# Kernel tuning notes

Hardware: AMD Instinct MI355X
Metric: run time of the kernel (lower is better)

## Reference

```python
import jax, jax.numpy as jnp
import numpy as np

B, S, H, I, E, TOPK, KS = 4, 4096, 1024, 512, 16, 2, 3


def setup_inputs() -> dict:
    key = jax.random.key(0)
    ks = jax.random.split(key, 9)
    sc = 0.02
    return {
        "hidden_states": jax.random.normal(ks[0], (B, S, H), dtype=jnp.float32),
        "router_w": jax.random.normal(ks[1], (H, E), dtype=jnp.float32) * sc,
        "router_bias": jnp.zeros((E,), dtype=jnp.float32),
        "expert_gate_w": jax.random.normal(ks[2], (E - 1, H, I), dtype=jnp.float32) * sc,
        "expert_up_w": jax.random.normal(ks[3], (E - 1, H, I), dtype=jnp.float32) * sc,
        "expert_down_w": jax.random.normal(ks[4], (E - 1, I, H), dtype=jnp.float32) * sc,
        "conv_w": jax.random.normal(ks[5], (I, H, KS), dtype=jnp.float32) * sc,
        "shared_up_w": jax.random.normal(ks[6], (H, I), dtype=jnp.float32) * sc,
        "shared_down_w": jax.random.normal(ks[7], (I, H), dtype=jnp.float32) * sc,
    }


def reference(hidden_states, router_w, router_bias, expert_gate_w, expert_up_w,
              expert_down_w, conv_w, shared_up_w, shared_down_w):
    b, s, h = hidden_states.shape
    flat = hidden_states.reshape(b * s, h)  # (T, H)

    # ---- Router (mlp type, temperature=1, no noise at eval) ----
    logits = (flat @ router_w).astype(jnp.float32) + router_bias  # (T, E)
    probs = jax.nn.softmax(logits, axis=-1)
    top_w, top_i = jax.lax.top_k(probs, TOPK)  # (T, K)
    norm_w = top_w / (jnp.sum(top_w, axis=-1, keepdims=True) + 1e-6)
    norm_w = norm_w.astype(hidden_states.dtype)
    # Dense combine weights (T, E): scatter top-k weights into expert slots
    combine = jnp.sum(jax.nn.one_hot(top_i, E, dtype=norm_w.dtype) * norm_w[..., None], axis=1)

    # ---- Routed experts: E-1 SwiGLU MLPs + 1 Identity (index E-1) ----
    routed = combine[:, E - 1:E] * flat  # identity expert contribution
    for e in range(E - 1):
        y = (jax.nn.silu(flat @ expert_gate_w[e]) * (flat @ expert_up_w[e])) @ expert_down_w[e]
        routed = routed + combine[:, e:e + 1] * y
    routed = routed.reshape(b, s, h)

    # ---- Shared expert: causal conv1d gate * up, then down ----
    x_ncw = jnp.transpose(hidden_states, (0, 2, 1))  # (B, H, S)
    gate = jax.lax.conv_general_dilated(
        x_ncw, conv_w, window_strides=(1,), padding=[(KS - 1, 0)],
        dimension_numbers=("NCW", "OIW", "NCW"))  # (B, I, S)
    gate = jnp.transpose(gate, (0, 2, 1))  # (B, S, I)
    shared = (jax.nn.silu(gate) * (hidden_states @ shared_up_w)) @ shared_down_w

    return shared + routed
```

## Files before the change

### kernel.cpp

```cpp
#include <hip/hip_runtime.h>

typedef unsigned short u16;
typedef __attribute__((ext_vector_type(4))) float f32x4;
using bf16x8 = __attribute__((ext_vector_type(8))) short;
typedef __attribute__((ext_vector_type(8))) unsigned short u16x8;
typedef __attribute__((ext_vector_type(4))) unsigned short u16x4;

#define GAS __attribute__((address_space(1)))
#define LAS __attribute__((address_space(3)))

__device__ __forceinline__ float bf2f(u16 u) {
  unsigned v = ((unsigned)u) << 16;
  float f;
  __builtin_memcpy(&f, &v, 4);
  return f;
}
__device__ __forceinline__ u16 f2bf(float f) {
  unsigned u;
  __builtin_memcpy(&u, &f, 4);
  u += 0x7fffu + ((u >> 16) & 1u);
  return (u16)(u >> 16);
}
__device__ __forceinline__ void llds16(const void* g, void* l) {
  __builtin_amdgcn_global_load_lds((const GAS unsigned*)g, (LAS unsigned*)l, 16, 0, 0);
}

__global__ void cvtx_k(const float* __restrict__ x, u16* __restrict__ xb) {
  const long i = (long)blockIdx.x * 256 + threadIdx.x;
  f32x4 v = *(const f32x4*)(x + i * 4);
  u16x4 r;
#pragma unroll
  for (int j = 0; j < 4; ++j) r[j] = f2bf(v[j]);
  *(u16x4*)(xb + i * 4) = r;
}

__global__ __launch_bounds__(256) void router_k(const float* __restrict__ x,
    const float* __restrict__ rw, const float* __restrict__ rb,
    int* __restrict__ topk_idx, float* __restrict__ topk_w, int* __restrict__ ib) {
  __shared__ float xs[4][32 * 65];
  __shared__ float wsm[4][32 * 16];
  __shared__ float part[4][64 * 17];
  __shared__ int cnt[16];
  const int tid = threadIdx.x;
  const int wv = __builtin_amdgcn_readfirstlane(tid >> 6);
  const int lane = tid & 63;
  const int tok0 = blockIdx.x * 64;
  const int rr = lane >> 3;
  const int c4 = (lane & 7) * 4;

  float acc[16];
#pragma unroll
  for (int e = 0; e < 16; ++e) acc[e] = 0.f;

  for (int c = 0; c < 8; ++c) {
    const int hb = wv * 256 + c * 32;
    {
      f32x4 wa = *(const f32x4*)(rw + hb * 16 + lane * 4);
      f32x4 wb = *(const f32x4*)(rw + hb * 16 + 256 + lane * 4);
      *(f32x4*)&wsm[wv][lane * 4] = wa;
      *(f32x4*)&wsm[wv][256 + lane * 4] = wb;
    }
#pragma unroll
    for (int i = 0; i < 8; ++i) {
      const int row = i * 8 + rr;
      f32x4 v = *(const f32x4*)(x + (long)(tok0 + row) * 1024 + hb + c4);
#pragma unroll
      for (int j = 0; j < 4; ++j) xs[wv][(c4 + j) * 65 + row] = v[j];
    }
    __syncthreads();
#pragma unroll
    for (int h = 0; h < 32; ++h) {
      const float xv = xs[wv][h * 65 + lane];
      const float* wrow = &wsm[wv][h * 16];
#pragma unroll
      for (int q = 0; q < 4; ++q) {
        f32x4 w4 = *(const f32x4*)(wrow + q * 4);
#pragma unroll
        for (int e = 0; e < 4; ++e) acc[q * 4 + e] += xv * w4[e];
      }
    }
    __syncthreads();
  }
#pragma unroll
  for (int e = 0; e < 16; ++e) part[wv][lane * 17 + e] = acc[e];
  if (tid < 16) cnt[tid] = 0;
  __syncthreads();
  if (tid < 64) {
    float p[16];
#pragma unroll
    for (int e = 0; e < 16; ++e)
      p[e] = part[0][tid * 17 + e] + part[1][tid * 17 + e] +
             part[2][tid * 17 + e] + part[3][tid * 17 + e] + rb[e];
    float mx = p[0];
#pragma unroll
    for (int e = 1; e < 16; ++e) mx = fmaxf(mx, p[e]);
    float sum = 0.f;
#pragma unroll
    for (int e = 0; e < 16; ++e) { p[e] = __expf(p[e] - mx); sum += p[e]; }
    int i0 = 0; float p0 = p[0];
    for (int e = 1; e < 16; ++e) if (p[e] > p0) { p0 = p[e]; i0 = e; }
    int i1 = -1; float p1 = -1.f;
    for (int e = 0; e < 16; ++e) if (e != i0 && p[e] > p1) { p1 = p[e]; i1 = e; }
    const float inv = 1.f / sum;
    p0 *= inv; p1 *= inv;
    const float d = p0 + p1 + 1e-6f;
    const int t = tok0 + tid;
    topk_idx[t * 2] = i0; topk_idx[t * 2 + 1] = i1;
    topk_w[t * 2] = p0 / d;
    topk_w[t * 2 + 1] = p1 / d;
    if (i0 < 15) atomicAdd(&cnt[i0], 1);
    if (i1 < 15) atomicAdd(&cnt[i1], 1);
  }
  __syncthreads();
  if (tid < 15 && cnt[tid] > 0) atomicAdd(&ib[tid], cnt[tid]);
}

__global__ void zero_k(int* __restrict__ ib) {
  if (threadIdx.x < 16) ib[threadIdx.x] = 0;
}

__global__ void scan_k(int* __restrict__ ib) {
  if (threadIdx.x != 0 || blockIdx.x != 0) return;
  int off = 0;
  for (int ee = 0; ee < 15; ++ee) { ib[16 + ee] = off; ib[32 + ee] = off; off += ib[ee]; }
  ib[16 + 15] = off;
  int nm = 0;
  for (int ee = 0; ee < 15; ++ee) {
    const int st = ib[16 + ee], en = ib[16 + ee + 1];
    for (int r = st; r < en; r += 128) {
      ib[64 + nm * 4] = ee; ib[64 + nm * 4 + 1] = r; ib[64 + nm * 4 + 2] = en; ++nm;
    }
  }
  ib[48] = nm;
}

__global__ __launch_bounds__(256) void scatter_k(const int* __restrict__ topk_idx,
                          const float* __restrict__ topk_w,
                          int* __restrict__ ib, int* __restrict__ tok_ids,
                          float* __restrict__ tok_w, int* __restrict__ slot_map) {
  __shared__ int cnt[16], base[16];
  const int tid = threadIdx.x;
  const int j = blockIdx.x * 256 + tid;
  if (tid < 16) cnt[tid] = 0;
  __syncthreads();
  const int e = topk_idx[j];
  int lo = 0;
  if (e < 15) lo = atomicAdd(&cnt[e], 1);
  __syncthreads();
  if (tid < 15 && cnt[tid] > 0) base[tid] = atomicAdd(&ib[32 + tid], cnt[tid]);
  __syncthreads();
  if (e < 15) {
    const int pos = base[e] + lo;
    tok_ids[pos] = j >> 1;
    tok_w[pos] = topk_w[j];
    slot_map[j] = pos;
  } else {
    slot_map[j] = -1;
  }
}

__global__ void transpose_k(const float* __restrict__ src, u16* __restrict__ dst, int R, int C) {
  __shared__ float tile[32][33];
  src += (long)blockIdx.z * R * C;
  dst += (long)blockIdx.z * R * C;
  const int c0 = blockIdx.x * 32, r0 = blockIdx.y * 32;
  const int tx = threadIdx.x & 31, ty = threadIdx.x >> 5;
#pragma unroll
  for (int i = ty; i < 32; i += 8) tile[i][tx] = src[(long)(r0 + i) * C + c0 + tx];
  __syncthreads();
#pragma unroll
  for (int i = ty; i < 32; i += 8) dst[(long)(c0 + i) * R + r0 + tx] = f2bf(tile[tx][i]);
}

__global__ void convt_k(const float* __restrict__ cw, u16* __restrict__ dst) {
  const int idx = blockIdx.x * 256 + threadIdx.x;
  if (idx >= 3 * 512 * 1024) return;
  const int k = idx >> 19;
  const int rem = idx & 524287;
  const int i = rem >> 10, h = rem & 1023;
  dst[idx] = f2bf(cw[i * 3072 + h * 3 + k]);
}

template<int V>
__global__ __launch_bounds__(256, 2)
void gemm_k(const u16* __restrict__ Abase, const u16* __restrict__ Bt0,
            const u16* __restrict__ Bt1, void* __restrict__ OUTv,
            const int* __restrict__ tbl, const int* __restrict__ nmt,
            const int* __restrict__ tok_ids, const float* __restrict__ tok_w,
            int K, int ldA, int ldOut) {
  __shared__ u16 lds[16384];
  u16* OUT = (u16*)OUTv;
  float* OUTF = (float*)OUTv;
  const int tid = threadIdx.x;
  const int wave = tid >> 6, lane = tid & 63;
  const int quad = lane >> 4, l16 = lane & 15;
  const int rA = tid >> 2;
  const int sub8 = (tid & 3) * 8;

  int e = 0, row0, row_end;
  if constexpr (V <= 1) {
    const int mt = blockIdx.x;
    if (mt >= *nmt) return;
    e = tbl[mt * 4]; row0 = tbl[mt * 4 + 1]; row_end = tbl[mt * 4 + 2];
  } else {
    row0 = blockIdx.x * 128; row_end = row0 + 128;
  }
  const int n0 = blockIdx.y * ((V == 0) ? 64 : 128);

  f32x4 acc[2][8];
#pragma unroll
  for (int i = 0; i < 2; ++i)
#pragma unroll
    for (int j = 0; j < 8; ++j) acc[i][j] = (f32x4){0.f, 0.f, 0.f, 0.f};

  const int aoff0 = (wave * 32 + l16) * 32 + quad * 8;
  const int aoff1 = aoff0 + 512;
  u16* ldsA0 = &lds[wave * 512];
  u16* ldsA1 = &lds[2048 + wave * 512];
  u16* ldsB0 = &lds[4096 + wave * 512];
  u16* ldsB1 = &lds[6144 + wave * 512];

  const int nph = (V == 3) ? 3 : 1;
  for (int ph = 0; ph < nph; ++ph) {
    const u16 *pA0, *pA1, *pB0, *pB1;
    bool zero0 = false;
    if constexpr (V == 0) {
      const int t0i = tok_ids[min(row0 + rA, row_end - 1)];
      const int t1i = tok_ids[min(row0 + rA + 64, row_end - 1)];
      pA0 = Abase + (long)t0i * 1024 + sub8;
      pA1 = Abase + (long)t1i * 1024 + sub8;
      pB0 = Bt0 + ((long)e * 512 + n0 + rA) * 1024 + sub8;
      pB1 = Bt1 + ((long)e * 512 + n0 + rA) * 1024 + sub8;
    } else if constexpr (V == 1) {
      pA0 = Abase + (long)min(row0 + rA, row_end - 1) * 512 + sub8;
      pA1 = Abase + (long)min(row0 + rA + 64, row_end - 1) * 512 + sub8;
      pB0 = Bt0 + ((long)e * 1024 + n0 + rA) * 512 + sub8;
      pB1 = Bt0 + ((long)e * 1024 + n0 + rA + 64) * 512 + sub8;
    } else if constexpr (V == 2 || V == 4) {
      pA0 = Abase + (long)(row0 + rA) * ldA + sub8;
      pA1 = Abase + (long)(row0 + rA + 64) * ldA + sub8;
      pB0 = Bt0 + (long)(n0 + rA) * K + sub8;
      pB1 = Bt0 + (long)(n0 + rA + 64) * K + sub8;
    } else {
      const int bb = row0 >> 12, s0 = row0 & 4095;
      const int si0 = s0 + ph - 2 + rA;
      zero0 = si0 < 0;
      pA0 = Abase + ((long)bb * 4096 + (si0 < 0 ? 0 : si0)) * 1024 + sub8;
      pA1 = Abase + ((long)bb * 4096 + (si0 + 64)) * 1024 + sub8;
      pB0 = Bt0 + (long)ph * 512 * 1024 + (long)(n0 + rA) * 1024 + sub8;
      pB1 = Bt0 + (long)ph * 512 * 1024 + (long)(n0 + rA + 64) * 1024 + sub8;
    }
    const int kIters = K / 32;
    for (int kb = 0; kb < kIters; ++kb) {
      u16x8 va0, va1;
      if constexpr (V == 3) {
        va0 = *(const u16x8*)pA0; pA0 += 32;
        va1 = *(const u16x8*)pA1; pA1 += 32;
        if (zero0) va0 = (u16x8){0, 0, 0, 0, 0, 0, 0, 0};
      }
      __syncthreads();
      if constexpr (V == 3) {
        *(u16x8*)&lds[rA * 32 + sub8] = va0;
        *(u16x8*)&lds[(rA + 64) * 32 + sub8] = va1;
      } else {
        llds16(pA0, ldsA0); pA0 += 32;
        llds16(pA1, ldsA1); pA1 += 32;
      }
      llds16(pB0, ldsB0); pB0 += 32;
      llds16(pB1, ldsB1); pB1 += 32;
      __syncthreads();
      bf16x8 a0 = *(const bf16x8*)&lds[aoff0];
      bf16x8 a1 = *(const bf16x8*)&lds[aoff1];
#pragma unroll
      for (int nt = 0; nt < 8; ++nt) {
        bf16x8 b = *(const bf16x8*)&lds[4096 + (nt * 16 + l16) * 32 + quad * 8];
        acc[0][nt] = __builtin_amdgcn_mfma_f32_16x16x32_bf16(a0, b, acc[0][nt], 0, 0, 0);
        acc[1][nt] = __builtin_amdgcn_mfma_f32_16x16x32_bf16(a1, b, acc[1][nt], 0, 0, 0);
      }
    }
  }
  __syncthreads();

  const int rbase = wave * 32;
  if constexpr (V == 0) {
#pragma unroll
    for (int mt = 0; mt < 2; ++mt)
#pragma unroll
      for (int r = 0; r < 4; ++r) {
        const int row = rbase + mt * 16 + quad * 4 + r;
#pragma unroll
        for (int nt = 0; nt < 4; ++nt) {
          float g = acc[mt][nt][r], u = acc[mt][nt + 4][r];
          float sg = g / (1.f + __expf(-g));
          lds[row * 64 + nt * 16 + l16] = f2bf(sg * u);
        }
      }
    __syncthreads();
#pragma unroll
    for (int i = 0; i < 4; ++i) {
      const int c = i * 256 + tid;
      const int row = c >> 3, s8 = (c & 7) * 8;
      const int slot = row0 + row;
      if (slot < row_end)
        *(u16x8*)(OUT + (long)slot * ldOut + n0 + s8) = *(const u16x8*)&lds[row * 64 + s8];
    }
  } else if constexpr (V == 1) {
#pragma unroll
    for (int mt = 0; mt < 2; ++mt)
#pragma unroll
      for (int r = 0; r < 4; ++r) {
        const int row = rbase + mt * 16 + quad * 4 + r;
        const float wgt = tok_w[min(row0 + row, row_end - 1)];
#pragma unroll
        for (int nt = 0; nt < 8; ++nt)
          lds[row * 128 + nt * 16 + l16] = f2bf(acc[mt][nt][r] * wgt);
      }
    __syncthreads();
#pragma unroll
    for (int i = 0; i < 8; ++i) {
      const int c = i * 256 + tid;
      const int row = c >> 4, s8 = (c & 15) * 8;
      const int slot = row0 + row;
      if (slot < row_end)
        *(u16x8*)(OUT + (long)slot * ldOut + n0 + s8) = *(const u16x8*)&lds[row * 128 + s8];
    }
  } else if constexpr (V == 2) {
#pragma unroll
    for (int mt = 0; mt < 2; ++mt)
#pragma unroll
      for (int r = 0; r < 4; ++r) {
        const int row = rbase + mt * 16 + quad * 4 + r;
#pragma unroll
        for (int nt = 0; nt < 8; ++nt)
          lds[row * 128 + nt * 16 + l16] = f2bf(acc[mt][nt][r]);
      }
    __syncthreads();
#pragma unroll
    for (int i = 0; i < 8; ++i) {
      const int c = i * 256 + tid;
      const int row = c >> 4, s8 = (c & 15) * 8;
      *(u16x8*)(OUT + (long)(row0 + row) * ldOut + n0 + s8) = *(const u16x8*)&lds[row * 128 + s8];
    }
  } else if constexpr (V == 3) {
#pragma unroll
    for (int mt = 0; mt < 2; ++mt)
#pragma unroll
      for (int r = 0; r < 4; ++r) {
        const int row = rbase + mt * 16 + quad * 4 + r;
#pragma unroll
        for (int nt = 0; nt < 8; ++nt) {
          float g = acc[mt][nt][r];
          lds[row * 128 + nt * 16 + l16] = f2bf(g / (1.f + __expf(-g)));
        }
      }
    __syncthreads();
#pragma unroll
    for (int i = 0; i < 8; ++i) {
      const int c = i * 256 + tid;
      const int row = c >> 4, s8 = (c & 15) * 8;
      const long o = (long)(row0 + row) * ldOut + n0 + s8;
      u16x8 sg8 = *(const u16x8*)&lds[row * 128 + s8];
      u16x8 up8 = *(const u16x8*)(OUT + o);
      u16x8 res;
#pragma unroll
      for (int j = 0; j < 8; ++j) res[j] = f2bf(bf2f(sg8[j]) * bf2f(up8[j]));
      *(u16x8*)(OUT + o) = res;
    }
  } else {
#pragma unroll
    for (int mt = 0; mt < 2; ++mt)
#pragma unroll
      for (int r = 0; r < 4; ++r) {
        const int row = row0 + rbase + mt * 16 + quad * 4 + r;
#pragma unroll
        for (int nt = 0; nt < 8; ++nt)
          OUTF[(long)row * ldOut + n0 + nt * 16 + l16] = acc[mt][nt][r];
      }
  }
}

__global__ void final_k(const float* __restrict__ x, const u16* __restrict__ Y,
                        const int* __restrict__ slot_map, const float* __restrict__ topk_w,
                        float* __restrict__ out) {
  const long idx = (long)blockIdx.x * 256 + threadIdx.x;
  const int t = (int)(idx >> 8), cc = ((int)idx & 255) * 4;
  const long ob = (long)t * 1024 + cc;
  f32x4 o = *(const f32x4*)(out + ob);
#pragma unroll
  for (int k2 = 0; k2 < 2; ++k2) {
    const int sm = slot_map[t * 2 + k2];
    if (sm >= 0) {
      u16x4 y = *(const u16x4*)(Y + (long)sm * 1024 + cc);
#pragma unroll
      for (int j = 0; j < 4; ++j) o[j] += bf2f(y[j]);
    } else {
      const float w = topk_w[t * 2 + k2];
      f32x4 xv = *(const f32x4*)(x + ob);
#pragma unroll
      for (int j = 0; j < 4; ++j) o[j] += w * xv[j];
    }
  }
  *(f32x4*)(out + ob) = o;
}

extern "C" void kernel_launch(void* const* d_in, const int* in_sizes, int n_in,
                              void* d_out, int out_size, void* d_ws, size_t ws_size,
                              hipStream_t stream) {
  (void)in_sizes; (void)n_in; (void)out_size; (void)ws_size;
  const float* x   = (const float*)d_in[0];
  const float* rw  = (const float*)d_in[1];
  const float* rb  = (const float*)d_in[2];
  const float* gw  = (const float*)d_in[3];
  const float* uw  = (const float*)d_in[4];
  const float* dw  = (const float*)d_in[5];
  const float* cw  = (const float*)d_in[6];
  const float* suw = (const float*)d_in[7];
  const float* sdw = (const float*)d_in[8];
  float* out = (float*)d_out;

  char* base = (char*)d_ws;
  size_t off = 0;
  auto alloc = [&](size_t b) { void* p = base + off; off = (off + b + 255) & ~(size_t)255; return p; };
  u16* xb     = (u16*)alloc(16777216ull * 2);
  u16* gate_t = (u16*)alloc(15ull * 512 * 1024 * 2);
  u16* up_t   = (u16*)alloc(15ull * 512 * 1024 * 2);
  u16* down_t = (u16*)alloc(15ull * 1024 * 512 * 2);
  u16* conv_t = (u16*)alloc(3ull * 512 * 1024 * 2);
  u16* sup_t  = (u16*)alloc(512ull * 1024 * 2);
  u16* sdn_t  = (u16*)alloc(512ull * 1024 * 2);
  u16* inter  = (u16*)alloc(32768ull * 512 * 2);
  u16* Y      = (u16*)alloc(32768ull * 1024 * 2);
  u16* UP     = (u16*)alloc(16384ull * 512 * 2);
  int*   topi    = (int*)alloc(32768 * 4);
  float* topw    = (float*)alloc(32768 * 4);
  int*   smap    = (int*)alloc(32768 * 4);
  int*   tok_ids = (int*)alloc(32768 * 4);
  float* tokw    = (float*)alloc(32768 * 4);
  int*   ib      = (int*)alloc(8192);

  zero_k<<<1, 64, 0, stream>>>(ib);
  cvtx_k<<<16384, 256, 0, stream>>>(x, xb);
  transpose_k<<<dim3(16, 32, 15), 256, 0, stream>>>(gw, gate_t, 1024, 512);
  transpose_k<<<dim3(16, 32, 15), 256, 0, stream>>>(uw, up_t, 1024, 512);
  transpose_k<<<dim3(32, 16, 15), 256, 0, stream>>>(dw, down_t, 512, 1024);
  transpose_k<<<dim3(16, 32, 1), 256, 0, stream>>>(suw, sup_t, 1024, 512);
  transpose_k<<<dim3(32, 16, 1), 256, 0, stream>>>(sdw, sdn_t, 512, 1024);
  convt_k<<<6144, 256, 0, stream>>>(cw, conv_t);
  router_k<<<256, 256, 0, stream>>>(x, rw, rb, topi, topw, ib);
  scan_k<<<1, 64, 0, stream>>>(ib);
  scatter_k<<<128, 256, 0, stream>>>(topi, topw, ib, tok_ids, tokw, smap);
  gemm_k<0><<<dim3(272, 8), 256, 0, stream>>>(xb, gate_t, up_t, inter, ib + 64, ib + 48,
                                              tok_ids, tokw, 1024, 1024, 512);
  gemm_k<1><<<dim3(272, 8), 256, 0, stream>>>(inter, down_t, nullptr, Y, ib + 64, ib + 48,
                                              nullptr, tokw, 512, 512, 1024);
  gemm_k<2><<<dim3(128, 4), 256, 0, stream>>>(xb, sup_t, nullptr, UP, nullptr, nullptr,
                                              nullptr, nullptr, 1024, 1024, 512);
  gemm_k<3><<<dim3(128, 4), 256, 0, stream>>>(xb, conv_t, nullptr, UP, nullptr, nullptr,
                                              nullptr, nullptr, 1024, 1024, 512);
  gemm_k<4><<<dim3(128, 8), 256, 0, stream>>>(UP, sdn_t, nullptr, out, nullptr, nullptr,
                                              nullptr, nullptr, 512, 512, 1024);
  final_k<<<16384, 256, 0, stream>>>(x, Y, smap, topw, out);
}
```

Baseline: 610.5 us.

## Double-buffer LDS tiles in the MFMA GEMM and XOR-swizzle K chunks

The GEMM main loop now ping-pongs between two LDS buffers. The next K-slice is loaded (global-to-LDS, or via registers for the conv variant) while MFMAs run on the current slice, which cuts the two barriers per iteration to one and lets load latency overlap compute. It also XOR-swizzles the 8-element K chunk position by row bits on both the global-load and LDS-read sides, to reduce LDS bank conflicts on the A/B fragment reads. In exchange it uses the full 32KB LDS array and adds some address arithmetic.

```diff
diff --git a/kernel.cpp b/kernel.cpp
--- a/kernel.cpp
+++ b/kernel.cpp
@@ -196,6 +196,7 @@
   const int quad = lane >> 4, l16 = lane & 15;
   const int rA = tid >> 2;
   const int sub8 = (tid & 3) * 8;
+  const int sub8s = ((tid & 3) ^ ((tid >> 3) & 3)) * 8;
 
   int e = 0, row0, row_end;
   if constexpr (V <= 1) {
@@ -213,73 +214,96 @@
 #pragma unroll
     for (int j = 0; j < 8; ++j) acc[i][j] = (f32x4){0.f, 0.f, 0.f, 0.f};
 
-  const int aoff0 = (wave * 32 + l16) * 32 + quad * 8;
+  const int swz8 = (((l16 >> 1) & 3) ^ quad) * 8;
+  const int aoff0 = (wave * 32 + l16) * 32 + swz8;
   const int aoff1 = aoff0 + 512;
-  u16* ldsA0 = &lds[wave * 512];
-  u16* ldsA1 = &lds[2048 + wave * 512];
-  u16* ldsB0 = &lds[4096 + wave * 512];
-  u16* ldsB1 = &lds[6144 + wave * 512];
+
+  int cur = 0;
+  u16x8 va0n, va1n;
 
   const int nph = (V == 3) ? 3 : 1;
+  const int kIters = K / 32;
   for (int ph = 0; ph < nph; ++ph) {
     const u16 *pA0, *pA1, *pB0, *pB1;
     bool zero0 = false;
     if constexpr (V == 0) {
       const int t0i = tok_ids[min(row0 + rA, row_end - 1)];
       const int t1i = tok_ids[min(row0 + rA + 64, row_end - 1)];
-      pA0 = Abase + (long)t0i * 1024 + sub8;
-      pA1 = Abase + (long)t1i * 1024 + sub8;
-      pB0 = Bt0 + ((long)e * 512 + n0 + rA) * 1024 + sub8;
-      pB1 = Bt1 + ((long)e * 512 + n0 + rA) * 1024 + sub8;
+      pA0 = Abase + (long)t0i * 1024 + sub8s;
+      pA1 = Abase + (long)t1i * 1024 + sub8s;
+      pB0 = Bt0 + ((long)e * 512 + n0 + rA) * 1024 + sub8s;
+      pB1 = Bt1 + ((long)e * 512 + n0 + rA) * 1024 + sub8s;
     } else if constexpr (V == 1) {
-      pA0 = Abase + (long)min(row0 + rA, row_end - 1) * 512 + sub8;
-      pA1 = Abase + (long)min(row0 + rA + 64, row_end - 1) * 512 + sub8;
-      pB0 = Bt0 + ((long)e * 1024 + n0 + rA) * 512 + sub8;
-      pB1 = Bt0 + ((long)e * 1024 + n0 + rA + 64) * 512 + sub8;
+      pA0 = Abase + (long)min(row0 + rA, row_end - 1) * 512 + sub8s;
+      pA1 = Abase + (long)min(row0 + rA + 64, row_end - 1) * 512 + sub8s;
+      pB0 = Bt0 + ((long)e * 1024 + n0 + rA) * 512 + sub8s;
+      pB1 = Bt0 + ((long)e * 1024 + n0 + rA + 64) * 512 + sub8s;
     } else if constexpr (V == 2 || V == 4) {
-      pA0 = Abase + (long)(row0 + rA) * ldA + sub8;
-      pA1 = Abase + (long)(row0 + rA + 64) * ldA + sub8;
-      pB0 = Bt0 + (long)(n0 + rA) * K + sub8;
-      pB1 = Bt0 + (long)(n0 + rA + 64) * K + sub8;
+      pA0 = Abase + (long)(row0 + rA) * ldA + sub8s;
+      pA1 = Abase + (long)(row0 + rA + 64) * ldA + sub8s;
+      pB0 = Bt0 + (long)(n0 + rA) * K + sub8s;
+      pB1 = Bt0 + (long)(n0 + rA + 64) * K + sub8s;
     } else {
       const int bb = row0 >> 12, s0 = row0 & 4095;
       const int si0 = s0 + ph - 2 + rA;
       zero0 = si0 < 0;
-      pA0 = Abase + ((long)bb * 4096 + (si0 < 0 ? 0 : si0)) * 1024 + sub8;
-      pA1 = Abase + ((long)bb * 4096 + (si0 + 64)) * 1024 + sub8;
-      pB0 = Bt0 + (long)ph * 512 * 1024 + (long)(n0 + rA) * 1024 + sub8;
-      pB1 = Bt0 + (long)ph * 512 * 1024 + (long)(n0 + rA + 64) * 1024 + sub8;
-    }
-    const int kIters = K / 32;
+      pA0 = Abase + ((long)bb * 4096 + (si0 < 0 ? 0 : si0)) * 1024 + sub8s;
+      pA1 = Abase + ((long)bb * 4096 + (si0 + 64)) * 1024 + sub8s;
+      pB0 = Bt0 + (long)ph * 512 * 1024 + (long)(n0 + rA) * 1024 + sub8s;
+      pB1 = Bt0 + (long)ph * 512 * 1024 + (long)(n0 + rA + 64) * 1024 + sub8s;
+    }
+
+    if constexpr (V == 3) {
+      va0n = *(const u16x8*)pA0; pA0 += 32;
+      va1n = *(const u16x8*)pA1; pA1 += 32;
+      if (zero0) va0n = (u16x8){0, 0, 0, 0, 0, 0, 0, 0};
+      *(u16x8*)&lds[cur + rA * 32 + sub8] = va0n;
+      *(u16x8*)&lds[cur + (rA + 64) * 32 + sub8] = va1n;
+    } else {
+      llds16(pA0, &lds[cur + wave * 512]); pA0 += 32;
+      llds16(pA1, &lds[cur + 2048 + wave * 512]); pA1 += 32;
+    }
+    llds16(pB0, &lds[cur + 4096 + wave * 512]); pB0 += 32;
+    llds16(pB1, &lds[cur + 6144 + wave * 512]); pB1 += 32;
+    __syncthreads();
+
     for (int kb = 0; kb < kIters; ++kb) {
-      u16x8 va0, va1;
+      const int nxt = cur ^ 8192;
+      const bool pre = (kb + 1 < kIters);
       if constexpr (V == 3) {
-        va0 = *(const u16x8*)pA0; pA0 += 32;
-        va1 = *(const u16x8*)pA1; pA1 += 32;
-        if (zero0) va0 = (u16x8){0, 0, 0, 0, 0, 0, 0, 0};
-      }
-      __syncthreads();
-      if constexpr (V == 3) {
-        *(u16x8*)&lds[rA * 32 + sub8] = va0;
-        *(u16x8*)&lds[(rA + 64) * 32 + sub8] = va1;
+        if (pre) {
+          llds16(pB0, &lds[nxt + 4096 + wave * 512]); pB0 += 32;
+          llds16(pB1, &lds[nxt + 6144 + wave * 512]); pB1 += 32;
+          va0n = *(const u16x8*)pA0; pA0 += 32;
+          va1n = *(const u16x8*)pA1; pA1 += 32;
+          if (zero0) va0n = (u16x8){0, 0, 0, 0, 0, 0, 0, 0};
+        }
       } else {
-        llds16(pA0, ldsA0); pA0 += 32;
-        llds16(pA1, ldsA1); pA1 += 32;
-      }
-      llds16(pB0, ldsB0); pB0 += 32;
-      llds16(pB1, ldsB1); pB1 += 32;
-      __syncthreads();
-      bf16x8 a0 = *(const bf16x8*)&lds[aoff0];
-      bf16x8 a1 = *(const bf16x8*)&lds[aoff1];
+        if (pre) {
+          llds16(pA0, &lds[nxt + wave * 512]); pA0 += 32;
+          llds16(pA1, &lds[nxt + 2048 + wave * 512]); pA1 += 32;
+          llds16(pB0, &lds[nxt + 4096 + wave * 512]); pB0 += 32;
+          llds16(pB1, &lds[nxt + 6144 + wave * 512]); pB1 += 32;
+        }
+      }
+      bf16x8 a0 = *(const bf16x8*)&lds[cur + aoff0];
+      bf16x8 a1 = *(const bf16x8*)&lds[cur + aoff1];
 #pragma unroll
       for (int nt = 0; nt < 8; ++nt) {
-        bf16x8 b = *(const bf16x8*)&lds[4096 + (nt * 16 + l16) * 32 + quad * 8];
+        bf16x8 b = *(const bf16x8*)&lds[cur + 4096 + (nt * 16 + l16) * 32 + swz8];
         acc[0][nt] = __builtin_amdgcn_mfma_f32_16x16x32_bf16(a0, b, acc[0][nt], 0, 0, 0);
         acc[1][nt] = __builtin_amdgcn_mfma_f32_16x16x32_bf16(a1, b, acc[1][nt], 0, 0, 0);
       }
-    }
-  }
-  __syncthreads();
+      if constexpr (V == 3) {
+        if (pre) {
+          *(u16x8*)&lds[nxt + rA * 32 + sub8] = va0n;
+          *(u16x8*)&lds[nxt + (rA + 64) * 32 + sub8] = va1n;
+        }
+      }
+      __syncthreads();
+      cur = nxt;
+    }
+  }
 
   const int rbase = wave * 32;
   if constexpr (V == 0) {
```

Result: no change. 603.2 us (-1.2%).
